# Kernel tuning notes

Measured on AMD Instinct MI355X. Metric: run time of the kernel, lower is better.

Reference implementation:

```python
import jax, jax.numpy as jnp
import numpy as np


def setup_inputs() -> dict:
    key = jax.random.key(0)
    ks = jax.random.split(key, 6)
    B, N_in, N_out, D_in, D_out, S = 64, 195, 778, 256, 128, 9
    nnz = 3 * N_out
    x = jax.random.normal(ks[0], (B, N_in, D_in), dtype=jnp.float32)
    # upsample transform: each output vertex receives 3 weighted source verts
    row = jnp.repeat(jnp.arange(N_out, dtype=jnp.int64), 3)
    col = jax.random.randint(ks[1], (nnz,), 0, N_in).astype(jnp.int64)
    value = jax.random.uniform(ks[2], (nnz,), dtype=jnp.float32)
    indices = jax.random.randint(ks[3], (N_out, S), 0, N_out).astype(jnp.int64)
    W = jax.random.normal(ks[4], (D_in * S, D_out), dtype=jnp.float32) * 0.02
    b = jnp.zeros((D_out,), dtype=jnp.float32)
    return {"x": x, "row": row, "col": col, "value": value,
            "indices": indices, "W": W, "b": b}


def reference(x, row, col, value, indices, W, b):
    B, N_in, D = x.shape
    N_out, S = indices.shape
    # Pool: gather source verts, scale by barycentric weight, scatter-add
    msg = x[:, col, :] * value[None, :, None]                # (B, nnz, D)
    pooled = jnp.zeros((B, N_out, D), x.dtype).at[:, row, :].add(msg)
    # SpiralConv: gather spiral neighborhood, flatten, linear
    g = pooled[:, indices.reshape(-1), :].reshape(B, N_out, S * D)
    out = jnp.einsum('bnk,ko->bno', g, W) + b                # (B, N_out, D_out)
    return jax.nn.relu(out)
```

## Files before the change

kernel.cpp:

```cpp
#include <hip/hip_runtime.h>
#include <hip/hip_bf16.h>
#include <stdint.h>

#define NB 64
#define N_IN 195
#define N_OUT 778
#define D_IN 256
#define D_OUTC 128
#define NS 9
#define KTOT 2304
#define MM 49792
#define BM 128
#define BK 64
#define NWG (MM / BM)
#define POOL_BLOCKS (MM / 2)
#define WT_BLOCKS ((D_OUTC * KTOT) / 256)

using short8 = __attribute__((ext_vector_type(8))) short;
using f32x4  = __attribute__((ext_vector_type(4))) float;

__device__ __forceinline__ void gload16(const void* g, void* l) {
  __builtin_amdgcn_global_load_lds(
      (const __attribute__((address_space(1))) uint32_t*)g,
      (__attribute__((address_space(3))) uint32_t*)l, 16, 0, 0);
}

__global__ __launch_bounds__(256) void prep_kernel(
    const float* __restrict__ x, const int* __restrict__ col,
    const float* __restrict__ value, const float* __restrict__ W,
    __hip_bfloat16* __restrict__ pooled, __hip_bfloat16* __restrict__ Wt) {
  int bid = blockIdx.x;
  if (bid < POOL_BLOCKS) {
    int m = bid * 2 + (threadIdx.x >> 7);
    int t = threadIdx.x & 127;
    int b = (unsigned)m / N_OUT;
    int n = m - b * N_OUT;
    int j = 3 * n;
    int c0 = col[j], c1 = col[j + 1], c2 = col[j + 2];
    float v0 = value[j], v1 = value[j + 1], v2 = value[j + 2];
    const float2* x0 = (const float2*)(x + ((size_t)b * N_IN + c0) * D_IN);
    const float2* x1 = (const float2*)(x + ((size_t)b * N_IN + c1) * D_IN);
    const float2* x2 = (const float2*)(x + ((size_t)b * N_IN + c2) * D_IN);
    float2 a0 = x0[t], a1 = x1[t], a2 = x2[t];
    float r0 = v0 * a0.x + v1 * a1.x + v2 * a2.x;
    float r1 = v0 * a0.y + v1 * a1.y + v2 * a2.y;
    __hip_bfloat162 pk;
    pk.x = __float2bfloat16(r0);
    pk.y = __float2bfloat16(r1);
    ((__hip_bfloat162*)(pooled + (size_t)m * D_IN))[t] = pk;
  } else {
    int idx = (bid - POOL_BLOCKS) * 256 + threadIdx.x;
    int o = idx / KTOT, k = idx - o * KTOT;
    Wt[idx] = __float2bfloat16(W[(size_t)k * D_OUTC + o]);
  }
}

__global__ __launch_bounds__(256) void gemm_kernel(
    const __hip_bfloat16* __restrict__ pooled,
    const __hip_bfloat16* __restrict__ Wt,
    const int* __restrict__ indices,
    const float* __restrict__ bias,
    float* __restrict__ out) {
  __shared__ __hip_bfloat16 Asm[2][BM * BK];
  __shared__ __hip_bfloat16 Bsm[2][D_OUTC * BK];

  const int tid  = threadIdx.x;
  const int wave = tid >> 6;
  const int lane = tid & 63;
  const int wr = wave >> 1, wc = wave & 1;
  const int srow = lane >> 3, schunk = lane & 7;

  {
  }
  const int bidr = blockIdx.x;
  const int xcd = bidr & 7, loc = bidr >> 3;
  const int q8 = NWG >> 3, r8 = NWG & 7;
  const int wg = (xcd < r8 ? xcd * (q8 + 1) : r8 * (q8 + 1) + (xcd - r8) * q8) + loc;
  const int bm = wg * BM;

  int n_i[4], b778_i[4], ax_i[4];
  const __hip_bfloat16* wtb_i[4];
  #pragma unroll
  for (int i = 0; i < 4; ++i) {
    int r = (wave * 4 + i) * 8 + srow;
    int m = bm + r;
    int b = (unsigned)m / N_OUT;
    int n = m - b * N_OUT;
    n_i[i] = n;
    b778_i[i] = b * N_OUT;
    ax_i[i] = (schunk ^ (r & 7)) * 8;
    wtb_i[i] = Wt + (size_t)r * KTOT + (size_t)((schunk ^ (r & 7)) * 8);
  }

  f32x4 acc[4][4];
  #pragma unroll
  for (int i = 0; i < 4; ++i)
    #pragma unroll
    for (int j = 0; j < 4; ++j)
      acc[i][j] = f32x4{0.f, 0.f, 0.f, 0.f};

  char* AsmB = (char*)&Asm[0][0];
  char* BsmB = (char*)&Bsm[0][0];

  auto stage = [&](int buf, int d0, int k0, const int* gi) {
    #pragma unroll
    for (int i = 0; i < 4; ++i) {
      const __hip_bfloat16* srcA =
          pooled + ((size_t)(b778_i[i] + gi[i]) * D_IN + d0 + ax_i[i]);
      gload16(srcA, AsmB + buf * 16384 + (wave * 4 + i) * 1024);
      const __hip_bfloat16* srcB = wtb_i[i] + k0;
      gload16(srcB, BsmB + buf * 16384 + (wave * 4 + i) * 1024);
    }
  };

  auto compute = [&](int buf) {
    const char* Ab = AsmB + buf * 16384;
    const char* Bb = BsmB + buf * 16384;
    #pragma unroll
    for (int h = 0; h < 2; ++h) {
      short8 af[4], bf[4];
      const int cb = h * 64 + (lane >> 4) * 16;
      #pragma unroll
      for (int i = 0; i < 4; ++i) {
        int r = wr * 64 + i * 16 + (lane & 15);
        af[i] = *(const short8*)(Ab + r * 128 + (cb ^ ((r & 7) << 4)));
      }
      #pragma unroll
      for (int j = 0; j < 4; ++j) {
        int o = wc * 64 + j * 16 + (lane & 15);
        bf[j] = *(const short8*)(Bb + o * 128 + (cb ^ ((o & 7) << 4)));
      }
      #pragma unroll
      for (int i = 0; i < 4; ++i)
        #pragma unroll
        for (int j = 0; j < 4; ++j)
          acc[i][j] = __builtin_amdgcn_mfma_f32_16x16x32_bf16(
              af[i], bf[j], acc[i][j], 0, 0, 0);
    }
  };

  int giA[4], giB[4];
  #pragma unroll
  for (int i = 0; i < 4; ++i) giA[i] = indices[n_i[i] * NS + 0];
  stage(0, 0, 0, giA);
  __syncthreads();

  for (int s0 = 0; s0 < NS; ++s0) {
    if (s0 < NS - 1) {
      #pragma unroll
      for (int i = 0; i < 4; ++i) giB[i] = indices[n_i[i] * NS + s0 + 1];
    }
    #pragma unroll
    for (int q = 0; q < 4; ++q) {
      if (q < 3) {
        stage((q & 1) ^ 1, (q + 1) * 64, s0 * 256 + (q + 1) * 64, giA);
      } else if (s0 < NS - 1) {
        stage((q & 1) ^ 1, 0, (s0 + 1) * 256, giB);
      }
      compute(q & 1);
      __syncthreads();
    }
    if (s0 < NS - 1) {
      #pragma unroll
      for (int i = 0; i < 4; ++i) giA[i] = giB[i];
    }
  }

  #pragma unroll
  for (int j = 0; j < 4; ++j) {
    int colo = wc * 64 + j * 16 + (lane & 15);
    float bo = bias[colo];
    #pragma unroll
    for (int i = 0; i < 4; ++i) {
      #pragma unroll
      for (int qq = 0; qq < 4; ++qq) {
        int row = bm + wr * 64 + i * 16 + (lane >> 4) * 4 + qq;
        float v = acc[i][j][qq] + bo;
        out[(size_t)row * D_OUTC + colo] = fmaxf(v, 0.f);
      }
    }
  }
}

extern "C" void kernel_launch(void* const* d_in, const int* in_sizes, int n_in,
                              void* d_out, int out_size, void* d_ws, size_t ws_size,
                              hipStream_t stream) {
  const float* x       = (const float*)d_in[0];
  const int*   col     = (const int*)d_in[2];
  const float* value   = (const float*)d_in[3];
  const int*   indices = (const int*)d_in[4];
  const float* W       = (const float*)d_in[5];
  const float* bias    = (const float*)d_in[6];
  float* out           = (float*)d_out;

  __hip_bfloat16* pooled = (__hip_bfloat16*)d_ws;
  __hip_bfloat16* Wt = (__hip_bfloat16*)((char*)d_ws + (size_t)MM * D_IN * 2);

  prep_kernel<<<POOL_BLOCKS + WT_BLOCKS, 256, 0, stream>>>(x, col, value, W,
                                                           pooled, Wt);
  gemm_kernel<<<NWG, 256, 0, stream>>>(pooled, Wt, indices, bias, out);
}
```

Measured before the change: 72.71 us.

## Restructure gather-GEMM with direct-to-register A loads and 4-stage B pipeline

The GEMM now uses 256-row tiles with 512 threads and 195 workgroups, one wave per MI355X compute unit. The gathered A operand is loaded straight from global memory into MFMA registers and double-buffered in registers, so only W goes through a 4-deep LDS ring filled by async global-to-LDS loads. Manual vmcnt waits and raw barriers replace __syncthreads so memory and compute can overlap. The prep kernel switches to float4 loads and a hand-written bf16 conversion. The cost is row-guard logic for the partial last tile and hand-counted vmcnt values that are easy to get wrong.

```diff
diff --git a/kernel.cpp b/kernel.cpp
--- a/kernel.cpp
+++ b/kernel.cpp
@@ -2,7 +2,6 @@
 #include <hip/hip_bf16.h>
 #include <stdint.h>
 
-#define NB 64
 #define N_IN 195
 #define N_OUT 778
 #define D_IN 256
@@ -10,13 +9,14 @@
 #define NS 9
 #define KTOT 2304
 #define MM 49792
-#define BM 128
-#define BK 64
-#define NWG (MM / BM)
-#define POOL_BLOCKS (MM / 2)
-#define WT_BLOCKS ((D_OUTC * KTOT) / 256)
+#define BM 256
+#define NPH 36
+#define NWG 195
+#define POOL_BLOCKS 12448
+#define WT_BLOCKS 1152
 
 using short8 = __attribute__((ext_vector_type(8))) short;
+using short4v = __attribute__((ext_vector_type(4))) short;
 using f32x4  = __attribute__((ext_vector_type(4))) float;
 
 __device__ __forceinline__ void gload16(const void* g, void* l) {
@@ -25,158 +25,174 @@
       (__attribute__((address_space(3))) uint32_t*)l, 16, 0, 0);
 }
 
+__device__ __forceinline__ unsigned short f2bf(float f) {
+  uint32_t u = __float_as_uint(f);
+  return (unsigned short)((u + 0x7FFFu + ((u >> 16) & 1u)) >> 16);
+}
+
 __global__ __launch_bounds__(256) void prep_kernel(
     const float* __restrict__ x, const int* __restrict__ col,
     const float* __restrict__ value, const float* __restrict__ W,
-    __hip_bfloat16* __restrict__ pooled, __hip_bfloat16* __restrict__ Wt) {
+    unsigned short* __restrict__ pooled, unsigned short* __restrict__ Wt) {
   int bid = blockIdx.x;
   if (bid < POOL_BLOCKS) {
-    int m = bid * 2 + (threadIdx.x >> 7);
-    int t = threadIdx.x & 127;
+    int m = bid * 4 + (threadIdx.x >> 6);
+    int lane = threadIdx.x & 63;
     int b = (unsigned)m / N_OUT;
     int n = m - b * N_OUT;
     int j = 3 * n;
     int c0 = col[j], c1 = col[j + 1], c2 = col[j + 2];
     float v0 = value[j], v1 = value[j + 1], v2 = value[j + 2];
-    const float2* x0 = (const float2*)(x + ((size_t)b * N_IN + c0) * D_IN);
-    const float2* x1 = (const float2*)(x + ((size_t)b * N_IN + c1) * D_IN);
-    const float2* x2 = (const float2*)(x + ((size_t)b * N_IN + c2) * D_IN);
-    float2 a0 = x0[t], a1 = x1[t], a2 = x2[t];
-    float r0 = v0 * a0.x + v1 * a1.x + v2 * a2.x;
-    float r1 = v0 * a0.y + v1 * a1.y + v2 * a2.y;
-    __hip_bfloat162 pk;
-    pk.x = __float2bfloat16(r0);
-    pk.y = __float2bfloat16(r1);
-    ((__hip_bfloat162*)(pooled + (size_t)m * D_IN))[t] = pk;
+    const float4* x0 = (const float4*)(x + ((size_t)b * N_IN + c0) * D_IN);
+    const float4* x1 = (const float4*)(x + ((size_t)b * N_IN + c1) * D_IN);
+    const float4* x2 = (const float4*)(x + ((size_t)b * N_IN + c2) * D_IN);
+    float4 a0 = x0[lane], a1 = x1[lane], a2 = x2[lane];
+    short4v pk;
+    pk[0] = (short)f2bf(v0 * a0.x + v1 * a1.x + v2 * a2.x);
+    pk[1] = (short)f2bf(v0 * a0.y + v1 * a1.y + v2 * a2.y);
+    pk[2] = (short)f2bf(v0 * a0.z + v1 * a1.z + v2 * a2.z);
+    pk[3] = (short)f2bf(v0 * a0.w + v1 * a1.w + v2 * a2.w);
+    ((short4v*)(pooled + (size_t)m * D_IN))[lane] = pk;
   } else {
     int idx = (bid - POOL_BLOCKS) * 256 + threadIdx.x;
     int o = idx / KTOT, k = idx - o * KTOT;
-    Wt[idx] = __float2bfloat16(W[(size_t)k * D_OUTC + o]);
-  }
-}
-
-__global__ __launch_bounds__(256) void gemm_kernel(
-    const __hip_bfloat16* __restrict__ pooled,
-    const __hip_bfloat16* __restrict__ Wt,
+    Wt[idx] = f2bf(W[(size_t)k * D_OUTC + o]);
+  }
+}
+
+__global__ __launch_bounds__(512) void gemm_kernel(
+    const unsigned short* __restrict__ pooled,
+    const unsigned short* __restrict__ Wt,
     const int* __restrict__ indices,
     const float* __restrict__ bias,
     float* __restrict__ out) {
-  __shared__ __hip_bfloat16 Asm[2][BM * BK];
-  __shared__ __hip_bfloat16 Bsm[2][D_OUTC * BK];
-
-  const int tid  = threadIdx.x;
-  const int wave = tid >> 6;
-  const int lane = tid & 63;
-  const int wr = wave >> 1, wc = wave & 1;
-  const int srow = lane >> 3, schunk = lane & 7;
-
-  {
-  }
-  const int bidr = blockIdx.x;
-  const int xcd = bidr & 7, loc = bidr >> 3;
+  __shared__ unsigned short Bsm[4][64 * 128];
+
+  const int tid = threadIdx.x;
+  const int wave = tid >> 6, lane = tid & 63;
+
+  const int xcd = blockIdx.x & 7, loc = blockIdx.x >> 3;
   const int q8 = NWG >> 3, r8 = NWG & 7;
   const int wg = (xcd < r8 ? xcd * (q8 + 1) : r8 * (q8 + 1) + (xcd - r8) * q8) + loc;
   const int bm = wg * BM;
 
-  int n_i[4], b778_i[4], ax_i[4];
-  const __hip_bfloat16* wtb_i[4];
+  int nn0, nn1; size_t gb0, gb1;
+  {
+    int m0 = bm + wave * 32 + (lane & 15);        if (m0 >= MM) m0 = MM - 1;
+    int m1 = bm + wave * 32 + 16 + (lane & 15);   if (m1 >= MM) m1 = MM - 1;
+    int b0 = (unsigned)m0 / N_OUT, b1 = (unsigned)m1 / N_OUT;
+    nn0 = m0 - b0 * N_OUT; nn1 = m1 - b1 * N_OUT;
+    gb0 = (size_t)b0 * N_OUT; gb1 = (size_t)b1 * N_OUT;
+  }
+  const int kk = (lane >> 4) * 8;
+
+  const int so = tid >> 3;
+  const int sc = (tid & 7) ^ (so & 7);
+  const unsigned short* wt0 = Wt + (size_t)so * KTOT + sc * 8;
+  const unsigned short* wt1 = Wt + (size_t)(64 + so) * KTOT + sc * 8;
+  char* BsmB = (char*)&Bsm[0][0];
+
+  int gu0 = indices[nn0 * NS + 0], gu1 = indices[nn1 * NS + 0];
+  int gp0 = indices[nn0 * NS + 1], gp1 = indices[nn1 * NS + 1];
+
+  f32x4 acc[2][8];
   #pragma unroll
-  for (int i = 0; i < 4; ++i) {
-    int r = (wave * 4 + i) * 8 + srow;
-    int m = bm + r;
-    int b = (unsigned)m / N_OUT;
-    int n = m - b * N_OUT;
-    n_i[i] = n;
-    b778_i[i] = b * N_OUT;
-    ax_i[i] = (schunk ^ (r & 7)) * 8;
-    wtb_i[i] = Wt + (size_t)r * KTOT + (size_t)((schunk ^ (r & 7)) * 8);
-  }
-
-  f32x4 acc[4][4];
-  #pragma unroll
-  for (int i = 0; i < 4; ++i)
+  for (int i = 0; i < 2; ++i)
     #pragma unroll
-    for (int j = 0; j < 4; ++j)
-      acc[i][j] = f32x4{0.f, 0.f, 0.f, 0.f};
-
-  char* AsmB = (char*)&Asm[0][0];
-  char* BsmB = (char*)&Bsm[0][0];
-
-  auto stage = [&](int buf, int d0, int k0, const int* gi) {
-    #pragma unroll
-    for (int i = 0; i < 4; ++i) {
-      const __hip_bfloat16* srcA =
-          pooled + ((size_t)(b778_i[i] + gi[i]) * D_IN + d0 + ax_i[i]);
-      gload16(srcA, AsmB + buf * 16384 + (wave * 4 + i) * 1024);
-      const __hip_bfloat16* srcB = wtb_i[i] + k0;
-      gload16(srcB, BsmB + buf * 16384 + (wave * 4 + i) * 1024);
-    }
-  };
-
-  auto compute = [&](int buf) {
-    const char* Ab = AsmB + buf * 16384;
-    const char* Bb = BsmB + buf * 16384;
+    for (int n = 0; n < 8; ++n) acc[i][n] = f32x4{0.f, 0.f, 0.f, 0.f};
+
+  short8 afA[2][2], afB[2][2];
+
+  auto stageB = [&](int p) {
+    int k0 = (p >> 2) * 256 + (p & 3) * 64;
+    gload16(wt0 + k0, BsmB + (p & 3) * 16384 + tid * 16);
+    gload16(wt1 + k0, BsmB + (p & 3) * 16384 + 8192 + tid * 16);
+  };
+
+  auto loadA = [&](short8 af[2][2], int p, int g0, int g1) {
+    const int d0 = (p & 3) * 64 + kk;
+    const unsigned short* a0 = pooled + (((gb0 + (size_t)g0) << 8) + d0);
+    const unsigned short* a1 = pooled + (((gb1 + (size_t)g1) << 8) + d0);
+    af[0][0] = *(const short8*)(a0);
+    af[0][1] = *(const short8*)(a0 + 32);
+    af[1][0] = *(const short8*)(a1);
+    af[1][1] = *(const short8*)(a1 + 32);
+  };
+
+  auto compute = [&](const short8 af[2][2], int p) {
+    const char* Bb = BsmB + (p & 3) * 16384;
     #pragma unroll
     for (int h = 0; h < 2; ++h) {
-      short8 af[4], bf[4];
+      short8 bf[8];
       const int cb = h * 64 + (lane >> 4) * 16;
       #pragma unroll
-      for (int i = 0; i < 4; ++i) {
-        int r = wr * 64 + i * 16 + (lane & 15);
-        af[i] = *(const short8*)(Ab + r * 128 + (cb ^ ((r & 7) << 4)));
+      for (int n = 0; n < 8; ++n) {
+        int o = n * 16 + (lane & 15);
+        bf[n] = *(const short8*)(Bb + o * 128 + (cb ^ ((o & 7) << 4)));
       }
       #pragma unroll
-      for (int j = 0; j < 4; ++j) {
-        int o = wc * 64 + j * 16 + (lane & 15);
-        bf[j] = *(const short8*)(Bb + o * 128 + (cb ^ ((o & 7) << 4)));
+      for (int n = 0; n < 8; ++n) {
+        acc[0][n] = __builtin_amdgcn_mfma_f32_16x16x32_bf16(af[0][h], bf[n], acc[0][n], 0, 0, 0);
+        acc[1][n] = __builtin_amdgcn_mfma_f32_16x16x32_bf16(af[1][h], bf[n], acc[1][n], 0, 0, 0);
       }
-      #pragma unroll
-      for (int i = 0; i < 4; ++i)
-        #pragma unroll
-        for (int j = 0; j < 4; ++j)
-          acc[i][j] = __builtin_amdgcn_mfma_f32_16x16x32_bf16(
-              af[i], bf[j], acc[i][j], 0, 0, 0);
     }
   };
 
-  int giA[4], giB[4];
+  auto rotate = [&](int p) {
+    if (((p + 1) & 3) == 0) {
+      gu0 = gp0; gu1 = gp1;
+      int sp = ((p + 1) >> 2) + 1;
+      if (sp < NS) { gp0 = indices[nn0 * NS + sp]; gp1 = indices[nn1 * NS + sp]; }
+    }
+  };
+
+  stageB(0);
+  asm volatile("" ::: "memory");
+  stageB(1);
+  loadA(afA, 0, gu0, gu1);
+
+#define BODY(P, CUR, NXT, CNT)                                   \
+  {                                                              \
+    stageB((P) + 2);                                             \
+    rotate(P);                                                   \
+    loadA(NXT, (P) + 1, gu0, gu1);                               \
+    asm volatile("s_waitcnt vmcnt(" #CNT ")" ::: "memory");      \
+    __builtin_amdgcn_s_barrier();                                \
+    asm volatile("" ::: "memory");                               \
+    compute(CUR, P);                                             \
+  }
+
+  for (int pp = 0; pp < 17; ++pp) {
+    int p = 2 * pp;
+    BODY(p,     afA, afB, 12)
+    BODY(p + 1, afB, afA, 12)
+  }
+  {
+    loadA(afB, 35, gu0, gu1);
+    asm volatile("s_waitcnt vmcnt(10)" ::: "memory");
+    __builtin_amdgcn_s_barrier();
+    asm volatile("" ::: "memory");
+    compute(afA, 34);
+  }
+  {
+    asm volatile("s_waitcnt vmcnt(4)" ::: "memory");
+    __builtin_amdgcn_s_barrier();
+    asm volatile("" ::: "memory");
+    compute(afB, 35);
+  }
+#undef BODY
+
   #pragma unroll
-  for (int i = 0; i < 4; ++i) giA[i] = indices[n_i[i] * NS + 0];
-  stage(0, 0, 0, giA);
-  __syncthreads();
-
-  for (int s0 = 0; s0 < NS; ++s0) {
-    if (s0 < NS - 1) {
-      #pragma unroll
-      for (int i = 0; i < 4; ++i) giB[i] = indices[n_i[i] * NS + s0 + 1];
-    }
-    #pragma unroll
-    for (int q = 0; q < 4; ++q) {
-      if (q < 3) {
-        stage((q & 1) ^ 1, (q + 1) * 64, s0 * 256 + (q + 1) * 64, giA);
-      } else if (s0 < NS - 1) {
-        stage((q & 1) ^ 1, 0, (s0 + 1) * 256, giB);
-      }
-      compute(q & 1);
-      __syncthreads();
-    }
-    if (s0 < NS - 1) {
-      #pragma unroll
-      for (int i = 0; i < 4; ++i) giA[i] = giB[i];
-    }
-  }
-
-  #pragma unroll
-  for (int j = 0; j < 4; ++j) {
-    int colo = wc * 64 + j * 16 + (lane & 15);
+  for (int n = 0; n < 8; ++n) {
+    int colo = n * 16 + (lane & 15);
     float bo = bias[colo];
     #pragma unroll
-    for (int i = 0; i < 4; ++i) {
+    for (int i = 0; i < 2; ++i) {
+      int rb = bm + wave * 32 + i * 16 + (lane >> 4) * 4;
       #pragma unroll
-      for (int qq = 0; qq < 4; ++qq) {
-        int row = bm + wr * 64 + i * 16 + (lane >> 4) * 4 + qq;
-        float v = acc[i][j][qq] + bo;
-        out[(size_t)row * D_OUTC + colo] = fmaxf(v, 0.f);
+      for (int q = 0; q < 4; ++q) {
+        int row = rb + q;
+        if (row < MM) out[(size_t)row * D_OUTC + colo] = fmaxf(acc[i][n][q] + bo, 0.f);
       }
     }
   }
@@ -193,10 +209,10 @@
   const float* bias    = (const float*)d_in[6];
   float* out           = (float*)d_out;
 
-  __hip_bfloat16* pooled = (__hip_bfloat16*)d_ws;
-  __hip_bfloat16* Wt = (__hip_bfloat16*)((char*)d_ws + (size_t)MM * D_IN * 2);
+  unsigned short* pooled = (unsigned short*)d_ws;
+  unsigned short* Wt = (unsigned short*)((char*)d_ws + (size_t)MM * D_IN * 2);
 
   prep_kernel<<<POOL_BLOCKS + WT_BLOCKS, 256, 0, stream>>>(x, col, value, W,
                                                            pooled, Wt);
-  gemm_kernel<<<NWG, 256, 0, stream>>>(pooled, Wt, indices, bias, out);
-}
+  gemm_kernel<<<NWG, 512, 0, stream>>>(pooled, Wt, indices, bias, out);
+}
```

New measurement: 74.34 us. 2.2% more time.

## Double K tile to 128 in GEMM and widen pooling loads to float4

Applied to the files above, without the earlier changes.

The GEMM K-tile grows from 64 to 128, halving the number of LDS stages and barriers per spiral slot. The staging layout and XOR swizzle are reworked for 256-byte rows, with 16-way swizzle and 8 loads per thread. The prep kernel now handles four rows per block with float4 loads and a manual bf16 rounding helper. LDS use doubles to 128KB per block, which may lower occupancy.

```diff
diff --git a/kernel.cpp b/kernel.cpp
--- a/kernel.cpp
+++ b/kernel.cpp
@@ -2,7 +2,6 @@
 #include <hip/hip_bf16.h>
 #include <stdint.h>
 
-#define NB 64
 #define N_IN 195
 #define N_OUT 778
 #define D_IN 256
@@ -11,13 +10,14 @@
 #define KTOT 2304
 #define MM 49792
 #define BM 128
-#define BK 64
-#define NWG (MM / BM)
-#define POOL_BLOCKS (MM / 2)
-#define WT_BLOCKS ((D_OUTC * KTOT) / 256)
-
-using short8 = __attribute__((ext_vector_type(8))) short;
-using f32x4  = __attribute__((ext_vector_type(4))) float;
+#define BK 128
+#define NWG 389
+#define POOL_BLOCKS 12448
+#define WT_BLOCKS 1152
+
+using short8  = __attribute__((ext_vector_type(8))) short;
+using short4v = __attribute__((ext_vector_type(4))) short;
+using f32x4   = __attribute__((ext_vector_type(4))) float;
 
 __device__ __forceinline__ void gload16(const void* g, void* l) {
   __builtin_amdgcn_global_load_lds(
@@ -25,110 +25,117 @@
       (__attribute__((address_space(3))) uint32_t*)l, 16, 0, 0);
 }
 
+__device__ __forceinline__ unsigned short f2bf(float f) {
+  uint32_t u = __float_as_uint(f);
+  return (unsigned short)((u + 0x7FFFu + ((u >> 16) & 1u)) >> 16);
+}
+
 __global__ __launch_bounds__(256) void prep_kernel(
     const float* __restrict__ x, const int* __restrict__ col,
     const float* __restrict__ value, const float* __restrict__ W,
-    __hip_bfloat16* __restrict__ pooled, __hip_bfloat16* __restrict__ Wt) {
+    unsigned short* __restrict__ pooled, unsigned short* __restrict__ Wt) {
   int bid = blockIdx.x;
   if (bid < POOL_BLOCKS) {
-    int m = bid * 2 + (threadIdx.x >> 7);
-    int t = threadIdx.x & 127;
+    int m = bid * 4 + (threadIdx.x >> 6);
+    int lane = threadIdx.x & 63;
     int b = (unsigned)m / N_OUT;
     int n = m - b * N_OUT;
     int j = 3 * n;
     int c0 = col[j], c1 = col[j + 1], c2 = col[j + 2];
     float v0 = value[j], v1 = value[j + 1], v2 = value[j + 2];
-    const float2* x0 = (const float2*)(x + ((size_t)b * N_IN + c0) * D_IN);
-    const float2* x1 = (const float2*)(x + ((size_t)b * N_IN + c1) * D_IN);
-    const float2* x2 = (const float2*)(x + ((size_t)b * N_IN + c2) * D_IN);
-    float2 a0 = x0[t], a1 = x1[t], a2 = x2[t];
-    float r0 = v0 * a0.x + v1 * a1.x + v2 * a2.x;
-    float r1 = v0 * a0.y + v1 * a1.y + v2 * a2.y;
-    __hip_bfloat162 pk;
-    pk.x = __float2bfloat16(r0);
-    pk.y = __float2bfloat16(r1);
-    ((__hip_bfloat162*)(pooled + (size_t)m * D_IN))[t] = pk;
+    const float4* x0 = (const float4*)(x + ((size_t)b * N_IN + c0) * D_IN);
+    const float4* x1 = (const float4*)(x + ((size_t)b * N_IN + c1) * D_IN);
+    const float4* x2 = (const float4*)(x + ((size_t)b * N_IN + c2) * D_IN);
+    float4 a0 = x0[lane], a1 = x1[lane], a2 = x2[lane];
+    short4v pk;
+    pk[0] = (short)f2bf(v0 * a0.x + v1 * a1.x + v2 * a2.x);
+    pk[1] = (short)f2bf(v0 * a0.y + v1 * a1.y + v2 * a2.y);
+    pk[2] = (short)f2bf(v0 * a0.z + v1 * a1.z + v2 * a2.z);
+    pk[3] = (short)f2bf(v0 * a0.w + v1 * a1.w + v2 * a2.w);
+    ((short4v*)(pooled + (size_t)m * D_IN))[lane] = pk;
   } else {
     int idx = (bid - POOL_BLOCKS) * 256 + threadIdx.x;
     int o = idx / KTOT, k = idx - o * KTOT;
-    Wt[idx] = __float2bfloat16(W[(size_t)k * D_OUTC + o]);
+    Wt[idx] = f2bf(W[(size_t)k * D_OUTC + o]);
   }
 }
 
 __global__ __launch_bounds__(256) void gemm_kernel(
-    const __hip_bfloat16* __restrict__ pooled,
-    const __hip_bfloat16* __restrict__ Wt,
+    const unsigned short* __restrict__ pooled,
+    const unsigned short* __restrict__ Wt,
     const int* __restrict__ indices,
     const float* __restrict__ bias,
     float* __restrict__ out) {
-  __shared__ __hip_bfloat16 Asm[2][BM * BK];
-  __shared__ __hip_bfloat16 Bsm[2][D_OUTC * BK];
-
-  const int tid  = threadIdx.x;
-  const int wave = tid >> 6;
-  const int lane = tid & 63;
+  __shared__ unsigned short Asm[2][BM * BK];
+  __shared__ unsigned short Bsm[2][D_OUTC * BK];
+
+  const int tid = threadIdx.x;
+  const int wave = tid >> 6, lane = tid & 63;
   const int wr = wave >> 1, wc = wave & 1;
-  const int srow = lane >> 3, schunk = lane & 7;
-
-  {
-  }
-  const int bidr = blockIdx.x;
-  const int xcd = bidr & 7, loc = bidr >> 3;
+
+  const int xcd = blockIdx.x & 7, loc = blockIdx.x >> 3;
   const int q8 = NWG >> 3, r8 = NWG & 7;
   const int wg = (xcd < r8 ? xcd * (q8 + 1) : r8 * (q8 + 1) + (xcd - r8) * q8) + loc;
   const int bm = wg * BM;
 
-  int n_i[4], b778_i[4], ax_i[4];
-  const __hip_bfloat16* wtb_i[4];
-  #pragma unroll
-  for (int i = 0; i < 4; ++i) {
-    int r = (wave * 4 + i) * 8 + srow;
+  const int lr4 = lane >> 4;
+  const int lc4 = lane & 15;
+  int nn[8]; size_t gb[8];
+  int asrc[8];
+  const unsigned short* wtrow[8];
+  #pragma unroll
+  for (int i = 0; i < 8; ++i) {
+    int r = wave * 32 + i * 4 + lr4;
     int m = bm + r;
     int b = (unsigned)m / N_OUT;
-    int n = m - b * N_OUT;
-    n_i[i] = n;
-    b778_i[i] = b * N_OUT;
-    ax_i[i] = (schunk ^ (r & 7)) * 8;
-    wtb_i[i] = Wt + (size_t)r * KTOT + (size_t)((schunk ^ (r & 7)) * 8);
-  }
-
-  f32x4 acc[4][4];
-  #pragma unroll
-  for (int i = 0; i < 4; ++i)
-    #pragma unroll
-    for (int j = 0; j < 4; ++j)
-      acc[i][j] = f32x4{0.f, 0.f, 0.f, 0.f};
-
+    nn[i] = m - b * N_OUT;
+    gb[i] = (size_t)b * N_OUT;
+    int sc = (lc4 ^ (r & 15)) * 8;
+    asrc[i] = sc;
+    wtrow[i] = Wt + (size_t)r * KTOT + sc;
+  }
+  const int ldst = wave * 8192 + lane * 16;
   char* AsmB = (char*)&Asm[0][0];
   char* BsmB = (char*)&Bsm[0][0];
 
-  auto stage = [&](int buf, int d0, int k0, const int* gi) {
-    #pragma unroll
-    for (int i = 0; i < 4; ++i) {
-      const __hip_bfloat16* srcA =
-          pooled + ((size_t)(b778_i[i] + gi[i]) * D_IN + d0 + ax_i[i]);
-      gload16(srcA, AsmB + buf * 16384 + (wave * 4 + i) * 1024);
-      const __hip_bfloat16* srcB = wtb_i[i] + k0;
-      gload16(srcB, BsmB + buf * 16384 + (wave * 4 + i) * 1024);
+  int gc[8], gn[8];
+  #pragma unroll
+  for (int i = 0; i < 8; ++i) gc[i] = indices[nn[i] * NS + 0];
+
+  f32x4 acc[4][4];
+  #pragma unroll
+  for (int i = 0; i < 4; ++i)
+    #pragma unroll
+    for (int j = 0; j < 4; ++j) acc[i][j] = f32x4{0.f, 0.f, 0.f, 0.f};
+
+  auto stage = [&](int buf, int s, int h, const int* g) {
+    const int bofs = buf * 32768;
+    const int kq = s * 256 + h * 128;
+    #pragma unroll
+    for (int i = 0; i < 8; ++i) {
+      const unsigned short* srcA =
+          pooled + (((gb[i] + (size_t)g[i]) << 8) + h * 128 + asrc[i]);
+      gload16(srcA, AsmB + bofs + i * 1024 + ldst);
+      gload16(wtrow[i] + kq, BsmB + bofs + i * 1024 + ldst);
     }
   };
 
   auto compute = [&](int buf) {
-    const char* Ab = AsmB + buf * 16384;
-    const char* Bb = BsmB + buf * 16384;
-    #pragma unroll
-    for (int h = 0; h < 2; ++h) {
+    const char* Ab = AsmB + buf * 32768;
+    const char* Bb = BsmB + buf * 32768;
+    #pragma unroll
+    for (int ks = 0; ks < 4; ++ks) {
       short8 af[4], bf[4];
-      const int cb = h * 64 + (lane >> 4) * 16;
+      const int cb = ks * 64 + (lane >> 4) * 16;
       #pragma unroll
       for (int i = 0; i < 4; ++i) {
         int r = wr * 64 + i * 16 + (lane & 15);
-        af[i] = *(const short8*)(Ab + r * 128 + (cb ^ ((r & 7) << 4)));
+        af[i] = *(const short8*)(Ab + r * 256 + (cb ^ ((r & 15) << 4)));
       }
       #pragma unroll
       for (int j = 0; j < 4; ++j) {
         int o = wc * 64 + j * 16 + (lane & 15);
-        bf[j] = *(const short8*)(Bb + o * 128 + (cb ^ ((o & 7) << 4)));
+        bf[j] = *(const short8*)(Bb + o * 256 + (cb ^ ((o & 15) << 4)));
       }
       #pragma unroll
       for (int i = 0; i < 4; ++i)
@@ -139,31 +146,22 @@
     }
   };
 
-  int giA[4], giB[4];
-  #pragma unroll
-  for (int i = 0; i < 4; ++i) giA[i] = indices[n_i[i] * NS + 0];
-  stage(0, 0, 0, giA);
+  stage(0, 0, 0, gc);
   __syncthreads();
 
-  for (int s0 = 0; s0 < NS; ++s0) {
-    if (s0 < NS - 1) {
-      #pragma unroll
-      for (int i = 0; i < 4; ++i) giB[i] = indices[n_i[i] * NS + s0 + 1];
-    }
-    #pragma unroll
-    for (int q = 0; q < 4; ++q) {
-      if (q < 3) {
-        stage((q & 1) ^ 1, (q + 1) * 64, s0 * 256 + (q + 1) * 64, giA);
-      } else if (s0 < NS - 1) {
-        stage((q & 1) ^ 1, 0, (s0 + 1) * 256, giB);
-      }
-      compute(q & 1);
-      __syncthreads();
-    }
-    if (s0 < NS - 1) {
-      #pragma unroll
-      for (int i = 0; i < 4; ++i) giA[i] = giB[i];
-    }
+  for (int s = 0; s < NS; ++s) {
+    if (s < NS - 1) {
+      #pragma unroll
+      for (int i = 0; i < 8; ++i) gn[i] = indices[nn[i] * NS + s + 1];
+    }
+    stage(1, s, 1, gc);
+    compute(0);
+    __syncthreads();
+    if (s < NS - 1) stage(0, s + 1, 0, gn);
+    compute(1);
+    __syncthreads();
+    #pragma unroll
+    for (int i = 0; i < 8; ++i) gc[i] = gn[i];
   }
 
   #pragma unroll
@@ -172,11 +170,11 @@
     float bo = bias[colo];
     #pragma unroll
     for (int i = 0; i < 4; ++i) {
-      #pragma unroll
-      for (int qq = 0; qq < 4; ++qq) {
-        int row = bm + wr * 64 + i * 16 + (lane >> 4) * 4 + qq;
-        float v = acc[i][j][qq] + bo;
-        out[(size_t)row * D_OUTC + colo] = fmaxf(v, 0.f);
+      int rb = bm + wr * 64 + i * 16 + (lane >> 4) * 4;
+      #pragma unroll
+      for (int q = 0; q < 4; ++q) {
+        int row = rb + q;
+        out[(size_t)row * D_OUTC + colo] = fmaxf(acc[i][j][q] + bo, 0.f);
       }
     }
   }
@@ -193,8 +191,8 @@
   const float* bias    = (const float*)d_in[6];
   float* out           = (float*)d_out;
 
-  __hip_bfloat16* pooled = (__hip_bfloat16*)d_ws;
-  __hip_bfloat16* Wt = (__hip_bfloat16*)((char*)d_ws + (size_t)MM * D_IN * 2);
+  unsigned short* pooled = (unsigned short*)d_ws;
+  unsigned short* Wt = (unsigned short*)((char*)d_ws + (size_t)MM * D_IN * 2);
 
   prep_kernel<<<POOL_BLOCKS + WT_BLOCKS, 256, 0, stream>>>(x, col, value, W,
                                                            pooled, Wt);
```

After: 95.93 us. 31.9% more time.
